# Performance work log

Hardware: AMD Instinct MI355X
Metric: run time of the kernel (lower is better)

The kernel has to match this reference:

```python
import jax, jax.numpy as jnp
import numpy as np

NEG_BIG = -9e15

def setup_inputs() -> dict:
    key = jax.random.key(0)
    k1, k2, k3, k4 = jax.random.split(key, 4)
    N, Fin, Fout = 8192, 128, 64
    x = jax.random.normal(k1, (N, Fin), dtype=jnp.float32)
    adj = jax.random.randint(k2, (N, N), 0, 2).astype(jnp.float32)
    W = jax.random.normal(k3, (Fin, Fout), dtype=jnp.float32) * (1.0 / np.sqrt(Fin))
    a = jax.random.normal(k4, (2 * Fout, 1), dtype=jnp.float32) * (1.0 / np.sqrt(2 * Fout))
    return {"x": x, "adj": adj, "W": W, "a": a}

def reference(x, adj, W, a):
    Fout = W.shape[1]
    Wh = x @ W                              # [N, Fout]
    Wh1 = Wh @ a[:Fout, :]                  # [N, 1]
    Wh2 = Wh @ a[Fout:, :]                  # [N, 1]
    e = jax.nn.leaky_relu(Wh1 + Wh2.T, negative_slope=0.2)  # [N, N]
    attention = jnp.where(adj > 0, e, NEG_BIG)
    attention = jax.nn.softmax(attention, axis=1)
    # dropout is identity in eval mode (training=False)
    h_prime = attention @ Wh                # [N, Fout]
    return jax.nn.elu(h_prime)
```

## Files before the change

### kernel.cpp

```cpp
#include <hip/hip_runtime.h>
#include <cstdint>
#include <cstddef>


#define NN   8192
#define FIN  128
#define FOUT 64
#define SJ   16
#define JCHUNK (NN / SJ)

typedef __attribute__((ext_vector_type(8))) short   short8;
typedef __attribute__((ext_vector_type(4))) float   f32x4;

#define LOG2E 1.44269504088896340736f
#define NTL(p) __builtin_nontemporal_load((const f32x4*)(p))

__global__ __launch_bounds__(256) void gat_phaseA(
    const float* __restrict__ x, const float* __restrict__ W,
    const float* __restrict__ a, unsigned short* __restrict__ WhP,
    float* __restrict__ Wh1, float* __restrict__ Wh2)
{
  const int wid  = threadIdx.x >> 6;
  const int lane = threadIdx.x & 63;
  const int row0 = (blockIdx.x * 4 + wid) * 4;
  const float a1 = a[lane];
  const float a2 = a[FOUT + lane];
  float acc[4] = {0.f, 0.f, 0.f, 0.f};
#pragma unroll 4
  for (int k = 0; k < FIN; k += 4) {
    float4 wv0 = make_float4(W[(k+0)*FOUT + lane], W[(k+1)*FOUT + lane],
                             W[(k+2)*FOUT + lane], W[(k+3)*FOUT + lane]);
#pragma unroll
    for (int r = 0; r < 4; ++r) {
      float4 xv = *(const float4*)(x + (row0 + r) * FIN + k);
      acc[r] = fmaf(xv.x, wv0.x, acc[r]);
      acc[r] = fmaf(xv.y, wv0.y, acc[r]);
      acc[r] = fmaf(xv.z, wv0.z, acc[r]);
      acc[r] = fmaf(xv.w, wv0.w, acc[r]);
    }
  }
  const int ft = lane >> 4, m = lane & 15;
#pragma unroll
  for (int r = 0; r < 4; ++r) {
    const int row = row0 + r;
    unsigned int u = __float_as_uint(acc[r]);
    unsigned int rb = (u + 0x7FFFu + ((u >> 16) & 1u)) >> 16;
    const int B0 = row >> 5, qq = (row >> 3) & 3, e = row & 7;
    WhP[(size_t)(B0 * 4 + ft) * 512 + (qq * 16 + m) * 8 + e] = (unsigned short)rb;
    float s1 = acc[r] * a1, s2 = acc[r] * a2;
#pragma unroll
    for (int off = 32; off; off >>= 1) {
      s1 += __shfl_xor(s1, off);
      s2 += __shfl_xor(s2, off);
    }
    if (lane == 0) { Wh1[row] = s1 * LOG2E; Wh2[row] = s2 * LOG2E; }
  }
}

#define AF_ONE(AF, AD0, AD1, W20, W21, WH1, RS)                          \
    _Pragma("unroll")                                                    \
    for (int e = 0; e < 4; ++e) {                                        \
      float t0 = (WH1) + (W20)[e];                                       \
      t0 = fmaxf(t0, 0.2f * t0);              \
      float p0 = exp2f(t0) * (AD0)[e];         \
      unsigned int pu0 = __float_as_uint(p0) & 0xFFFF0000u;              \
      RS += __uint_as_float(pu0);            \
      AF[e] = (short)(pu0 >> 16);                                        \
      float t1 = (WH1) + (W21)[e];                                       \
      t1 = fmaxf(t1, 0.2f * t1);                                         \
      float p1 = exp2f(t1) * (AD1)[e];                                   \
      unsigned int pu1 = __float_as_uint(p1) & 0xFFFF0000u;              \
      RS += __uint_as_float(pu1);                                        \
      AF[4 + e] = (short)(pu1 >> 16);                                    \
    }

#define GAT_BODY(AD00, AD01, AD10, AD11, W2C0, W2C1, BC0, BC1, BC2, BC3, \
                 W2N0, W2N1, BN0, BN1, BN2, BN3, JN1, BLK1, JN2)         \
  {                                                                      \
    W2N0 = *(const f32x4*)(w2base + (JN1));                              \
    W2N1 = *(const f32x4*)(w2base + (JN1) + 4);                          \
    BN0  = *(const short8*)(wpbase + (size_t)(BLK1) * 2048);             \
    BN1  = *(const short8*)(wpbase + (size_t)(BLK1) * 2048 + 512);       \
    BN2  = *(const short8*)(wpbase + (size_t)(BLK1) * 2048 + 1024);      \
    BN3  = *(const short8*)(wpbase + (size_t)(BLK1) * 2048 + 1536);      \
    __builtin_amdgcn_sched_barrier(0);                                   \
    short8 af0, af1;                                                     \
    AF_ONE(af0, AD00, AD01, W2C0, W2C1, wh1_0, rsum0);                   \
    AF_ONE(af1, AD10, AD11, W2C0, W2C1, wh1_1, rsum1);                   \
    AD00 = NTL(adjrow0 + (JN2)); AD01 = NTL(adjrow0 + (JN2) + 4);        \
    AD10 = NTL(adjrow1 + (JN2)); AD11 = NTL(adjrow1 + (JN2) + 4);        \
    __builtin_amdgcn_sched_barrier(0);                                   \
    c00 = __builtin_amdgcn_mfma_f32_16x16x32_bf16(af0, BC0, c00, 0,0,0); \
    c01 = __builtin_amdgcn_mfma_f32_16x16x32_bf16(af0, BC1, c01, 0,0,0); \
    c02 = __builtin_amdgcn_mfma_f32_16x16x32_bf16(af0, BC2, c02, 0,0,0); \
    c03 = __builtin_amdgcn_mfma_f32_16x16x32_bf16(af0, BC3, c03, 0,0,0); \
    c10 = __builtin_amdgcn_mfma_f32_16x16x32_bf16(af1, BC0, c10, 0,0,0); \
    c11 = __builtin_amdgcn_mfma_f32_16x16x32_bf16(af1, BC1, c11, 0,0,0); \
    c12 = __builtin_amdgcn_mfma_f32_16x16x32_bf16(af1, BC2, c12, 0,0,0); \
    c13 = __builtin_amdgcn_mfma_f32_16x16x32_bf16(af1, BC3, c13, 0,0,0); \
  }

__global__ __launch_bounds__(256, 3) void gat_phaseB(
    const float* __restrict__ adj, const unsigned short* __restrict__ WhP,
    const float* __restrict__ Wh1, const float* __restrict__ Wh2,
    float* __restrict__ accbuf, float* __restrict__ denbuf, int nslices)
{
  const int wid  = threadIdx.x >> 6;
  const int lane = threadIdx.x & 63;
  const int jc   = blockIdx.x % SJ;
  const int rg   = (blockIdx.x / SJ) * 4 + wid;
  const int m = lane & 15;
  const int q = lane >> 4;
  const int r0 = rg * 32 + m;
  const int r1 = r0 + 16;
  const float wh1_0 = Wh1[r0];
  const float wh1_1 = Wh1[r1];
  const float* adjrow0 = adj + (size_t)r0 * NN + q * 8;
  const float* adjrow1 = adj + (size_t)r1 * NN + q * 8;
  const unsigned short* wpbase = WhP + (size_t)(jc * 16) * 2048 + lane * 8;
  const float* w2base = Wh2 + q * 8;

  f32x4 c00 = {0.f,0.f,0.f,0.f}, c01 = c00, c02 = c00, c03 = c00;
  f32x4 c10 = c00, c11 = c00, c12 = c00, c13 = c00;
  float rsum0 = 0.f, rsum1 = 0.f;

  const int jbeg = jc * JCHUNK;

  f32x4 w2A0, w2A1, w2B0, w2B1;
  short8 bA0, bA1, bA2, bA3, bB0, bB1, bB2, bB3;
  f32x4 adA00, adA01, adA10, adA11;
  f32x4 adB00, adB01, adB10, adB11;

  w2A0 = *(const f32x4*)(w2base + jbeg);
  w2A1 = *(const f32x4*)(w2base + jbeg + 4);
  bA0  = *(const short8*)(wpbase);
  bA1  = *(const short8*)(wpbase + 512);
  bA2  = *(const short8*)(wpbase + 1024);
  bA3  = *(const short8*)(wpbase + 1536);
  adA00 = NTL(adjrow0 + jbeg);      adA01 = NTL(adjrow0 + jbeg + 4);
  adA10 = NTL(adjrow1 + jbeg);      adA11 = NTL(adjrow1 + jbeg + 4);
  adB00 = NTL(adjrow0 + jbeg + 32); adB01 = NTL(adjrow0 + jbeg + 36);
  adB10 = NTL(adjrow1 + jbeg + 32); adB11 = NTL(adjrow1 + jbeg + 36);

#pragma unroll
  for (int bb = 0; bb < 16; bb += 2) {
    const int b1 = (bb + 1 < 16) ? bb + 1 : 0;
    const int b2 = (bb + 2 < 16) ? bb + 2 : 0;
    const int b3 = (bb + 3 < 16) ? bb + 3 : 0;
    GAT_BODY(adA00, adA01, adA10, adA11, w2A0, w2A1, bA0, bA1, bA2, bA3,
             w2B0, w2B1, bB0, bB1, bB2, bB3, jbeg + b1 * 32, b1, jbeg + b2 * 32);
    GAT_BODY(adB00, adB01, adB10, adB11, w2B0, w2B1, bB0, bB1, bB2, bB3,
             w2A0, w2A1, bA0, bA1, bA2, bA3, jbeg + b2 * 32, b2, jbeg + b3 * 32);
  }

  rsum0 += __shfl_xor(rsum0, 16);
  rsum0 += __shfl_xor(rsum0, 32);
  rsum1 += __shfl_xor(rsum1, 16);
  rsum1 += __shfl_xor(rsum1, 32);

  const int slice = (nslices > 1) ? jc : 0;
  float* accout = accbuf + (size_t)slice * (NN * FOUT);
  float* denout = denbuf + slice * NN;
  f32x4 cc0[4] = {c00, c01, c02, c03};
  f32x4 cc1[4] = {c10, c11, c12, c13};
  if (nslices > 1) {
    if (q == 0) { denout[r0] = rsum0; denout[r1] = rsum1; }
#pragma unroll
    for (int ft = 0; ft < 4; ++ft)
#pragma unroll
      for (int r = 0; r < 4; ++r) {
        accout[(rg * 32 +      q * 4 + r) * FOUT + ft * 16 + m] = cc0[ft][r];
        accout[(rg * 32 + 16 + q * 4 + r) * FOUT + ft * 16 + m] = cc1[ft][r];
      }
  } else {
    if (q == 0) { atomicAdd(&denout[r0], rsum0); atomicAdd(&denout[r1], rsum1); }
#pragma unroll
    for (int ft = 0; ft < 4; ++ft)
#pragma unroll
      for (int r = 0; r < 4; ++r) {
        atomicAdd(&accout[(rg * 32 +      q * 4 + r) * FOUT + ft * 16 + m], cc0[ft][r]);
        atomicAdd(&accout[(rg * 32 + 16 + q * 4 + r) * FOUT + ft * 16 + m], cc1[ft][r]);
      }
  }
}

__global__ __launch_bounds__(256) void gat_phaseC(
    const float* __restrict__ accbuf, const float* __restrict__ denbuf,
    float* __restrict__ out, int nslices)
{
  const int idx4 = blockIdx.x * 256 + threadIdx.x;
  const int idx  = idx4 * 4;
  const int row  = idx >> 6;
  f32x4 s = {0.f, 0.f, 0.f, 0.f};
  float d = 0.f;
  for (int sl = 0; sl < nslices; ++sl) {
    f32x4 v = *(const f32x4*)(accbuf + (size_t)sl * (NN * FOUT) + idx);
    s += v;
    d += denbuf[sl * NN + row];
  }
  float inv = 1.0f / d;
  f32x4 o;
#pragma unroll
  for (int e = 0; e < 4; ++e) {
    float v = s[e] * inv;
    o[e] = (v > 0.f) ? v : expm1f(v);
  }
  *(f32x4*)(out + idx) = o;
}

extern "C" void kernel_launch(void* const* d_in, const int* in_sizes, int n_in,
                              void* d_out, int out_size, void* d_ws, size_t ws_size,
                              hipStream_t stream)
{
  const float* x   = (const float*)d_in[0];
  const float* adj = (const float*)d_in[1];
  const float* W   = (const float*)d_in[2];
  const float* a   = (const float*)d_in[3];
  float* out = (float*)d_out;

  const size_t accEl = (size_t)NN * FOUT;
  const size_t whpBytes = (size_t)(NN / 32) * 4 * 512 * 2;
  const size_t roomyBytes = (size_t)SJ * accEl * 4 + (size_t)SJ * NN * 4
                          + (size_t)NN * 8 + whpBytes;
  const int nslices = (ws_size >= roomyBytes) ? SJ : 1;

  char* ws = (char*)d_ws;
  float* accbuf = (float*)ws;
  size_t off = (size_t)nslices * accEl * 4;
  float* denbuf = (float*)(ws + off); off += (size_t)nslices * NN * 4;
  float* Wh1 = (float*)(ws + off);    off += (size_t)NN * 4;
  float* Wh2 = (float*)(ws + off);    off += (size_t)NN * 4;
  unsigned short* WhP = (unsigned short*)(ws + off);

  if (nslices == 1)
    hipMemsetAsync(accbuf, 0, accEl * 4 + (size_t)NN * 4, stream);

  gat_phaseA<<<NN / 16, 256, 0, stream>>>(x, W, a, WhP, Wh1, Wh2);
  gat_phaseB<<<((NN / 32) * SJ) / 4, 256, 0, stream>>>(adj, WhP, Wh1, Wh2,
                                                       accbuf, denbuf, nslices);
  gat_phaseC<<<(NN * FOUT) / 4 / 256, 256, 0, stream>>>(accbuf, denbuf, out, nslices);
}
```

Measured before the change: 394.5 us.

## Stage WhP panel in LDS per block instead of per-wave global prefetch

```diff
diff --git a/kernel.cpp b/kernel.cpp
--- a/kernel.cpp
+++ b/kernel.cpp
@@ -74,33 +74,32 @@
       AF[4 + e] = (short)(pu1 >> 16);                                    \
     }
 
-#define GAT_BODY(AD00, AD01, AD10, AD11, W2C0, W2C1, BC0, BC1, BC2, BC3, \
-                 W2N0, W2N1, BN0, BN1, BN2, BN3, JN1, BLK1, JN2)         \
+#define GAT_BODY(AD00, AD01, AD10, AD11, W2C0, W2C1, W2N0, W2N1,         \
+                 BLK, JN1, JN2)                                          \
   {                                                                      \
+    const unsigned short* pb = panel + (BLK) * 2048 + lane * 8;          \
+    short8 b0 = *(const short8*)(pb);                                    \
+    short8 b1 = *(const short8*)(pb + 512);                              \
+    short8 b2 = *(const short8*)(pb + 1024);                             \
+    short8 b3 = *(const short8*)(pb + 1536);                             \
     W2N0 = *(const f32x4*)(w2base + (JN1));                              \
     W2N1 = *(const f32x4*)(w2base + (JN1) + 4);                          \
-    BN0  = *(const short8*)(wpbase + (size_t)(BLK1) * 2048);             \
-    BN1  = *(const short8*)(wpbase + (size_t)(BLK1) * 2048 + 512);       \
-    BN2  = *(const short8*)(wpbase + (size_t)(BLK1) * 2048 + 1024);      \
-    BN3  = *(const short8*)(wpbase + (size_t)(BLK1) * 2048 + 1536);      \
-    __builtin_amdgcn_sched_barrier(0);                                   \
     short8 af0, af1;                                                     \
     AF_ONE(af0, AD00, AD01, W2C0, W2C1, wh1_0, rsum0);                   \
     AF_ONE(af1, AD10, AD11, W2C0, W2C1, wh1_1, rsum1);                   \
     AD00 = NTL(adjrow0 + (JN2)); AD01 = NTL(adjrow0 + (JN2) + 4);        \
     AD10 = NTL(adjrow1 + (JN2)); AD11 = NTL(adjrow1 + (JN2) + 4);        \
-    __builtin_amdgcn_sched_barrier(0);                                   \
-    c00 = __builtin_amdgcn_mfma_f32_16x16x32_bf16(af0, BC0, c00, 0,0,0); \
-    c01 = __builtin_amdgcn_mfma_f32_16x16x32_bf16(af0, BC1, c01, 0,0,0); \
-    c02 = __builtin_amdgcn_mfma_f32_16x16x32_bf16(af0, BC2, c02, 0,0,0); \
-    c03 = __builtin_amdgcn_mfma_f32_16x16x32_bf16(af0, BC3, c03, 0,0,0); \
-    c10 = __builtin_amdgcn_mfma_f32_16x16x32_bf16(af1, BC0, c10, 0,0,0); \
-    c11 = __builtin_amdgcn_mfma_f32_16x16x32_bf16(af1, BC1, c11, 0,0,0); \
-    c12 = __builtin_amdgcn_mfma_f32_16x16x32_bf16(af1, BC2, c12, 0,0,0); \
-    c13 = __builtin_amdgcn_mfma_f32_16x16x32_bf16(af1, BC3, c13, 0,0,0); \
-  }
-
-__global__ __launch_bounds__(256, 3) void gat_phaseB(
+    c00 = __builtin_amdgcn_mfma_f32_16x16x32_bf16(af0, b0, c00, 0,0,0);  \
+    c01 = __builtin_amdgcn_mfma_f32_16x16x32_bf16(af0, b1, c01, 0,0,0);  \
+    c02 = __builtin_amdgcn_mfma_f32_16x16x32_bf16(af0, b2, c02, 0,0,0);  \
+    c03 = __builtin_amdgcn_mfma_f32_16x16x32_bf16(af0, b3, c03, 0,0,0);  \
+    c10 = __builtin_amdgcn_mfma_f32_16x16x32_bf16(af1, b0, c10, 0,0,0);  \
+    c11 = __builtin_amdgcn_mfma_f32_16x16x32_bf16(af1, b1, c11, 0,0,0);  \
+    c12 = __builtin_amdgcn_mfma_f32_16x16x32_bf16(af1, b2, c12, 0,0,0);  \
+    c13 = __builtin_amdgcn_mfma_f32_16x16x32_bf16(af1, b3, c13, 0,0,0);  \
+  }
+
+__global__ __launch_bounds__(256, 2) void gat_phaseB(
     const float* __restrict__ adj, const unsigned short* __restrict__ WhP,
     const float* __restrict__ Wh1, const float* __restrict__ Wh2,
     float* __restrict__ accbuf, float* __restrict__ denbuf, int nslices)
@@ -117,8 +116,17 @@
   const float wh1_1 = Wh1[r1];
   const float* adjrow0 = adj + (size_t)r0 * NN + q * 8;
   const float* adjrow1 = adj + (size_t)r1 * NN + q * 8;
-  const unsigned short* wpbase = WhP + (size_t)(jc * 16) * 2048 + lane * 8;
   const float* w2base = Wh2 + q * 8;
+
+  __shared__ __align__(16) unsigned short panel[16 * 2048];
+  {
+    const f32x4* src = (const f32x4*)(WhP + (size_t)jc * 16 * 2048) + threadIdx.x;
+    f32x4* dst = (f32x4*)panel + threadIdx.x;
+#pragma unroll
+    for (int k = 0; k < 16; ++k)
+      dst[k * 256] = src[k * 256];
+  }
+  __syncthreads();
 
   f32x4 c00 = {0.f,0.f,0.f,0.f}, c01 = c00, c02 = c00, c03 = c00;
   f32x4 c10 = c00, c11 = c00, c12 = c00, c13 = c00;
@@ -127,16 +135,11 @@
   const int jbeg = jc * JCHUNK;
 
   f32x4 w2A0, w2A1, w2B0, w2B1;
-  short8 bA0, bA1, bA2, bA3, bB0, bB1, bB2, bB3;
   f32x4 adA00, adA01, adA10, adA11;
   f32x4 adB00, adB01, adB10, adB11;
 
   w2A0 = *(const f32x4*)(w2base + jbeg);
   w2A1 = *(const f32x4*)(w2base + jbeg + 4);
-  bA0  = *(const short8*)(wpbase);
-  bA1  = *(const short8*)(wpbase + 512);
-  bA2  = *(const short8*)(wpbase + 1024);
-  bA3  = *(const short8*)(wpbase + 1536);
   adA00 = NTL(adjrow0 + jbeg);      adA01 = NTL(adjrow0 + jbeg + 4);
   adA10 = NTL(adjrow1 + jbeg);      adA11 = NTL(adjrow1 + jbeg + 4);
   adB00 = NTL(adjrow0 + jbeg + 32); adB01 = NTL(adjrow0 + jbeg + 36);
@@ -144,13 +147,13 @@
 
 #pragma unroll
   for (int bb = 0; bb < 16; bb += 2) {
-    const int b1 = (bb + 1 < 16) ? bb + 1 : 0;
-    const int b2 = (bb + 2 < 16) ? bb + 2 : 0;
-    const int b3 = (bb + 3 < 16) ? bb + 3 : 0;
-    GAT_BODY(adA00, adA01, adA10, adA11, w2A0, w2A1, bA0, bA1, bA2, bA3,
-             w2B0, w2B1, bB0, bB1, bB2, bB3, jbeg + b1 * 32, b1, jbeg + b2 * 32);
-    GAT_BODY(adB00, adB01, adB10, adB11, w2B0, w2B1, bB0, bB1, bB2, bB3,
-             w2A0, w2A1, bA0, bA1, bA2, bA3, jbeg + b2 * 32, b2, jbeg + b3 * 32);
+    const int j1 = ((bb + 1) & 15) * 32;
+    const int j2 = ((bb + 2) & 15) * 32;
+    const int j3 = ((bb + 3) & 15) * 32;
+    GAT_BODY(adA00, adA01, adA10, adA11, w2A0, w2A1, w2B0, w2B1,
+             bb,     jbeg + j1, jbeg + j2);
+    GAT_BODY(adB00, adB01, adB10, adB11, w2B0, w2B1, w2A0, w2A1,
+             bb + 1, jbeg + j2, jbeg + j3);
   }
 
   rsum0 += __shfl_xor(rsum0, 16);
```

Result: faster. 378.3 us (-4.1%).
